# Optimization experiments

Measured on AMD Instinct MI355X. Metric: run time of the kernel, lower is better.

Reference implementation:

```python
import jax, jax.numpy as jnp
import numpy as np

WS = (8, 8)  # window_size
NUM_HEADS = 6


def _relative_position_index(ws):
    ch, cw = np.arange(ws[0]), np.arange(ws[1])
    coords = np.stack(np.meshgrid(ch, cw, indexing='ij'))  # [2, Wh, Ww]
    cf = coords.reshape(2, -1)  # [2, N]
    rel = cf[:, :, None] - cf[:, None, :]  # [2, N, N]
    rel = rel.transpose(1, 2, 0).astype(np.int64)
    rel[:, :, 0] += ws[0] - 1
    rel[:, :, 1] += ws[1] - 1
    rel[:, :, 0] *= 2 * ws[1] - 1
    return rel.sum(-1)  # [N, N]

_RPI = jnp.asarray(_relative_position_index(WS))  # [64, 64] int


def setup_inputs() -> dict:
    key = jax.random.key(0)
    ks = jax.random.split(key, 6)
    B_, N, C = 4096, WS[0] * WS[1], 192
    return {
        'x': jax.random.normal(ks[0], (B_, N, C), jnp.float32),
        'qkv_w': jax.random.normal(ks[1], (3 * C, C), jnp.float32) * 0.02,
        'qkv_b': jax.random.normal(ks[2], (3 * C,), jnp.float32) * 0.02,
        'proj_w': jax.random.normal(ks[3], (C, C), jnp.float32) * 0.02,
        'proj_b': jax.random.normal(ks[4], (C,), jnp.float32) * 0.02,
        'rpb_table': jax.random.normal(ks[5], ((2 * WS[0] - 1) * (2 * WS[1] - 1), NUM_HEADS), jnp.float32) * 0.02,
    }


def reference(x, qkv_w, qkv_b, proj_w, proj_b, rpb_table):
    B_, N, C = x.shape
    H = NUM_HEADS
    D = C // H
    scale = D ** (-0.5)
    # qkv: torch Linear -> x @ W^T + b
    qkv = (x @ qkv_w.T + qkv_b).reshape(B_, N, 3, H, D)
    qkv = jnp.transpose(qkv, (2, 0, 3, 1, 4))  # [3, B_, H, N, D]
    q, k, v = qkv[0] * scale, qkv[1], qkv[2]
    attn = jnp.einsum('bhnd,bhmd->bhnm', q, k)  # [B_, H, N, N]
    bias = rpb_table[_RPI]  # [N, N, H]
    attn = attn + jnp.transpose(bias, (2, 0, 1))[None]  # broadcast over B_
    attn = jax.nn.softmax(attn, axis=-1)
    out = jnp.einsum('bhnm,bhmd->bnhd', attn, v).reshape(B_, N, C)
    return out @ proj_w.T + proj_b
```

## Files before the change

kernel.cpp:

```cpp
#include <hip/hip_runtime.h>
#include <hip/hip_bf16.h>

typedef short bf16x8 __attribute__((ext_vector_type(8)));
typedef float f32x4 __attribute__((ext_vector_type(4)));
typedef unsigned int u32;
typedef unsigned int u32x2 __attribute__((ext_vector_type(2)));

#define MFMA16 __builtin_amdgcn_mfma_f32_16x16x32_bf16
#define SCALE 0.17677669529663687f

#define OS_OFF 395520
#define WS_NEED (395520 + 100663296)

__device__ __forceinline__ unsigned short f2b(float x) {
  u32 u = __float_as_uint(x);
  u = (u + 0x7FFFu + ((u >> 16) & 1u)) >> 16;
  return (unsigned short)u;
}
__device__ __forceinline__ u32 pk2(float a, float b) {
  __hip_bfloat162 h = __float22bfloat162_rn(float2{a, b});
  return *(u32*)&h;
}
__device__ __forceinline__ uint2 pk4(f32x4 v) {
  return make_uint2(pk2(v[0], v[1]), pk2(v[2], v[3]));
}

__device__ __forceinline__ bf16x8 xpose(f32x4 a0, f32x4 a1) {
  u32 s0 = pk2(a0[0], a0[1]);
  u32 s1 = pk2(a0[2], a0[3]);
  u32 s2 = pk2(a1[0], a1[1]);
  u32 s3 = pk2(a1[2], a1[3]);
  u32x2 r0 = __builtin_amdgcn_permlane16_swap(s0, s2, false, false);
  u32x2 r1 = __builtin_amdgcn_permlane16_swap(s1, s3, false, false);
  union {
    u32 w[4];
    bf16x8 v;
  } u;
  u.w[0] = r0[0];
  u.w[1] = r1[0];
  u.w[2] = r0[1];
  u.w[3] = r1[1];
  return u.v;
}

__global__ void prep_kernel(const float* __restrict__ qkv_w, const float* __restrict__ qkv_b,
                            const float* __restrict__ proj_w, const float* __restrict__ rpb,
                            unsigned short* __restrict__ wqkv, unsigned short* __restrict__ wproj,
                            float* __restrict__ biasar, float* __restrict__ bq) {
  int i0 = blockIdx.x * blockDim.x + threadIdx.x;
  int stride = gridDim.x * blockDim.x;
  for (int i = i0; i < 576 * 192; i += stride) {
    float v = qkv_w[i];
    if (i < 192 * 192) v *= SCALE;
    wqkv[i] = f2b(v);
  }
  for (int i = i0; i < 192 * 192; i += stride) wproj[i] = f2b(proj_w[i]);
  for (int i = i0; i < 576; i += stride) {
    float v = qkv_b[i];
    if (i < 192) v *= SCALE;
    bq[i] = v;
  }
  for (int i = i0; i < 6 * 16 * 64 * 4; i += stride) {
    int r = i & 3;
    int lane = (i >> 2) & 63;
    int fid = (i >> 8) & 15;
    int h = i >> 12;
    int mt = fid >> 2, nt = fid & 3;
    int m = mt * 16 + (lane >> 4) * 4 + r;
    int n = nt * 16 + (lane & 15);
    int idx = ((n >> 3) - (m >> 3) + 7) * 15 + ((n & 7) - (m & 7) + 7);
    biasar[i] = rpb[idx * 6 + h];
  }
}

__global__ void __launch_bounds__(384, 4) win_attn6(
    const float* __restrict__ x, const unsigned short* __restrict__ wqkv,
    const float* __restrict__ biasar, const float* __restrict__ bq,
    unsigned short* __restrict__ osout) {
  __shared__ __align__(16) char smem[50176];
  const int bid = blockIdx.x;
  const int b = bid >> 1;
  const int hg = bid & 1;
  const int tid = threadIdx.x;
  const int wv = tid >> 6;
  const int hl = wv >> 1;
  const int head = hg * 3 + hl;
  const int half = wv & 1;
  const int lane = tid & 63;
  const int g = lane >> 4;
  const int c = lane & 15;
  char* xs = smem;
  char* exch = smem + 25600;

  {
    const float4* src = (const float4*)(x + (size_t)b * 12288) + tid;
    char* wdst = xs + (tid / 48) * 400 + (tid % 48) * 8;
#pragma unroll
    for (int it = 0; it < 8; ++it) {
      float4 v = src[it * 384];
      *(uint2*)(wdst + it * 3200) = make_uint2(pk2(v.x, v.y), pk2(v.z, v.w));
    }
  }
  __syncthreads();

  const char* xr = xs + c * 400 + g * 16;
#define XF(tt, kt) (*(const bf16x8*)(xr + (tt) * 6400 + (kt) * 64))

  bf16x8 qb[2];
  {
    const unsigned short* wq0 = wqkv + (size_t)(head * 32 + c) * 192 + 8 * g;
    const unsigned short* wq1 = wq0 + 16 * 192;
    f32x4 bq0 = *(const f32x4*)(bq + head * 32 + 4 * g);
    f32x4 bq1 = *(const f32x4*)(bq + head * 32 + 16 + 4 * g);
    f32x4 a00 = bq0, a01 = bq0, a10 = bq1, a11 = bq1;
#pragma unroll
    for (int kt = 0; kt < 6; ++kt) {
      bf16x8 w0 = *(const bf16x8*)(wq0 + kt * 32);
      bf16x8 w1 = *(const bf16x8*)(wq1 + kt * 32);
      bf16x8 x0 = XF(half * 2 + 0, kt);
      bf16x8 x1 = XF(half * 2 + 1, kt);
      a00 = MFMA16(w0, x0, a00, 0, 0, 0);
      a10 = MFMA16(w1, x0, a10, 0, 0, 0);
      a01 = MFMA16(w0, x1, a01, 0, 0, 0);
      a11 = MFMA16(w1, x1, a11, 0, 0, 0);
    }
    qb[0] = xpose(a00, a10);
    qb[1] = xpose(a01, a11);
  }

  bf16x8 ka[4], va[2][2];
  {
    char* ew = exch + hl * 8192 + half * 4096 + lane * 16;
    if (half == 0) {
      const unsigned short* wk0 = wqkv + (size_t)(192 + head * 32 + c) * 192 + 8 * g;
      const unsigned short* wk1 = wk0 + 16 * 192;
      f32x4 bk0 = *(const f32x4*)(bq + 192 + head * 32 + 4 * g);
      f32x4 bk1 = *(const f32x4*)(bq + 192 + head * 32 + 16 + 4 * g);
      f32x4 acc[2][4];
#pragma unroll
      for (int tt = 0; tt < 4; ++tt) {
        acc[0][tt] = bk0;
        acc[1][tt] = bk1;
      }
#pragma unroll
      for (int kt = 0; kt < 6; ++kt) {
        bf16x8 w0 = *(const bf16x8*)(wk0 + kt * 32);
        bf16x8 w1 = *(const bf16x8*)(wk1 + kt * 32);
#pragma unroll
        for (int tt = 0; tt < 4; ++tt) {
          bf16x8 xf = XF(tt, kt);
          acc[0][tt] = MFMA16(w0, xf, acc[0][tt], 0, 0, 0);
          acc[1][tt] = MFMA16(w1, xf, acc[1][tt], 0, 0, 0);
        }
      }
#pragma unroll
      for (int mt = 0; mt < 4; ++mt) {
        ka[mt] = xpose(acc[0][mt], acc[1][mt]);
        *(bf16x8*)(ew + mt * 1024) = ka[mt];
      }
    } else {
      const unsigned short* wv0 = wqkv + (size_t)(384 + head * 32 + c) * 192 + 8 * g;
      const unsigned short* wv1 = wv0 + 16 * 192;
      float bv0 = bq[384 + head * 32 + c];
      float bv1 = bq[384 + head * 32 + 16 + c];
      f32x4 acc[4][2];
#pragma unroll
      for (int tt = 0; tt < 4; ++tt) {
        acc[tt][0] = f32x4{bv0, bv0, bv0, bv0};
        acc[tt][1] = f32x4{bv1, bv1, bv1, bv1};
      }
#pragma unroll
      for (int kt = 0; kt < 6; ++kt) {
        bf16x8 w0 = *(const bf16x8*)(wv0 + kt * 32);
        bf16x8 w1 = *(const bf16x8*)(wv1 + kt * 32);
#pragma unroll
        for (int tt = 0; tt < 4; ++tt) {
          bf16x8 xf = XF(tt, kt);
          acc[tt][0] = MFMA16(xf, w0, acc[tt][0], 0, 0, 0);
          acc[tt][1] = MFMA16(xf, w1, acc[tt][1], 0, 0, 0);
        }
      }
#pragma unroll
      for (int dt = 0; dt < 2; ++dt)
#pragma unroll
        for (int kh = 0; kh < 2; ++kh) {
          va[dt][kh] = xpose(acc[2 * kh][dt], acc[2 * kh + 1][dt]);
          *(bf16x8*)(ew + (dt * 2 + kh) * 1024) = va[dt][kh];
        }
    }
  }
  __syncthreads();
  {
    const char* er = exch + hl * 8192 + (half ^ 1) * 4096 + lane * 16;
    if (half == 0) {
#pragma unroll
      for (int f = 0; f < 4; ++f) va[f >> 1][f & 1] = *(const bf16x8*)(er + f * 1024);
    } else {
#pragma unroll
      for (int f = 0; f < 4; ++f) ka[f] = *(const bf16x8*)(er + f * 1024);
    }
  }

  bf16x8 pbf[2][2];
  float linv[2];
  {
    const f32x4* bias4 = (const f32x4*)biasar + (size_t)(head * 16 + half * 2) * 64 + lane;
    f32x4 s[4][2];
#pragma unroll
    for (int mt = 0; mt < 4; ++mt)
#pragma unroll
      for (int n2 = 0; n2 < 2; ++n2)
        s[mt][n2] = MFMA16(ka[mt], qb[n2], bias4[(mt * 4 + n2) * 64], 0, 0, 0);
#pragma unroll
    for (int n2 = 0; n2 < 2; ++n2) {
      float mx = fmaxf(fmaxf(fmaxf(s[0][n2][0], s[0][n2][1]), fmaxf(s[0][n2][2], s[0][n2][3])),
                       fmaxf(fmaxf(s[1][n2][0], s[1][n2][1]), fmaxf(s[1][n2][2], s[1][n2][3])));
      mx = fmaxf(mx, fmaxf(fmaxf(fmaxf(s[2][n2][0], s[2][n2][1]), fmaxf(s[2][n2][2], s[2][n2][3])),
                           fmaxf(fmaxf(s[3][n2][0], s[3][n2][1]), fmaxf(s[3][n2][2], s[3][n2][3]))));
      mx = fmaxf(mx, __shfl_xor(mx, 16));
      mx = fmaxf(mx, __shfl_xor(mx, 32));
      float sum = 0.0f;
#pragma unroll
      for (int mt = 0; mt < 4; ++mt)
#pragma unroll
        for (int r = 0; r < 4; ++r) {
          float e = __expf(s[mt][n2][r] - mx);
          s[mt][n2][r] = e;
          sum += e;
        }
      sum += __shfl_xor(sum, 16);
      sum += __shfl_xor(sum, 32);
      linv[n2] = 1.0f / sum;
    }
#pragma unroll
    for (int n2 = 0; n2 < 2; ++n2) {
      pbf[0][n2] = xpose(s[0][n2], s[1][n2]);
      pbf[1][n2] = xpose(s[2][n2], s[3][n2]);
    }
  }

  f32x4 o[2][2];
#pragma unroll
  for (int dt = 0; dt < 2; ++dt)
#pragma unroll
    for (int n2 = 0; n2 < 2; ++n2) o[dt][n2] = (f32x4)0.0f;
#pragma unroll
  for (int mh = 0; mh < 2; ++mh)
#pragma unroll
    for (int n2 = 0; n2 < 2; ++n2)
#pragma unroll
      for (int dt = 0; dt < 2; ++dt) o[dt][n2] = MFMA16(va[dt][mh], pbf[mh][n2], o[dt][n2], 0, 0, 0);

  uint2* dst = (uint2*)osout + ((size_t)((b * 6 + head) * 2 + half) * 4) * 64 + lane;
#pragma unroll
  for (int dt = 0; dt < 2; ++dt)
#pragma unroll
    for (int n2 = 0; n2 < 2; ++n2) {
#pragma unroll
      for (int r = 0; r < 4; ++r) o[dt][n2][r] *= linv[n2];
      dst[(dt * 2 + n2) * 64] = pk4(o[dt][n2]);
    }
}

__global__ void __launch_bounds__(256, 4) proj_kernel(
    const unsigned short* __restrict__ osin, const unsigned short* __restrict__ wproj,
    const float* __restrict__ proj_b, float* __restrict__ out) {
  __shared__ __align__(16) char smem[24576];
  const int b = blockIdx.x;
  const int tid = threadIdx.x;
  const int w = tid >> 6;
  const int lane = tid & 63;
  const int g = lane >> 4;
  const int c = lane & 15;

  {
    const uint2* src = (const uint2*)osin + (size_t)b * 3072;
#pragma unroll
    for (int it = 0; it < 12; ++it) {
      int i = tid + it * 256;
      int ls = i & 63;
      int f = (i >> 6) & 3;
      int unit = i >> 8;
      int head = unit >> 1, half = unit & 1;
      int dt = f >> 1, n2 = f & 1;
      int tok = half * 32 + n2 * 16 + (ls & 15);
      int d0 = head * 32 + dt * 16 + 4 * (ls >> 4);
      uint2 v = src[i];
      *(uint2*)(smem + tok * 384 + (((d0 >> 3) ^ (tok & 7)) << 4) + (d0 & 7) * 2) = v;
    }
  }
  __syncthreads();

  f32x4 acc[4][3];
#pragma unroll
  for (int mt = 0; mt < 4; ++mt)
#pragma unroll
    for (int ft = 0; ft < 3; ++ft) acc[mt][ft] = (f32x4)0.0f;
#pragma unroll
  for (int kt = 0; kt < 6; ++kt) {
    bf16x8 wf[3];
#pragma unroll
    for (int ft = 0; ft < 3; ++ft)
      wf[ft] = *(const bf16x8*)(wproj + (size_t)(w * 48 + ft * 16 + c) * 192 + kt * 32 + 8 * g);
#pragma unroll
    for (int mt = 0; mt < 4; ++mt) {
      bf16x8 of = *(const bf16x8*)(smem + (mt * 16 + c) * 384 + (((kt * 4 + g) ^ (c & 7)) << 4));
#pragma unroll
      for (int ft = 0; ft < 3; ++ft) acc[mt][ft] = MFMA16(of, wf[ft], acc[mt][ft], 0, 0, 0);
    }
  }
  float* outb = out + (size_t)b * 12288;
#pragma unroll
  for (int ft = 0; ft < 3; ++ft) {
    float pbv = proj_b[w * 48 + ft * 16 + c];
#pragma unroll
    for (int mt = 0; mt < 4; ++mt)
#pragma unroll
      for (int r = 0; r < 4; ++r)
        outb[(mt * 16 + 4 * g + r) * 192 + w * 48 + ft * 16 + c] = acc[mt][ft][r] + pbv;
  }
}

#define XFRAGOLD(tt, kt) \
  (*(const bf16x8*)(xs + ((tt) * 16 + c) * 384 + ((((kt) * 4 + g) ^ (c & 7)) << 4)))

__global__ void __launch_bounds__(384, 3) win_attn(
    const float* __restrict__ x, const unsigned short* __restrict__ wqkv,
    const unsigned short* __restrict__ wproj, const float* __restrict__ biasar,
    const float* __restrict__ bq, const float* __restrict__ proj_b, float* __restrict__ out) {
  __shared__ __align__(16) char smem[24576];
  const int b = blockIdx.x;
  const int tid = threadIdx.x;
  const int w = tid >> 6;
  const int lane = tid & 63;
  const int g = lane >> 4;
  const int c = lane & 15;
  char* xs = smem;

  {
    const float* xb = x + (size_t)b * 12288;
#pragma unroll
    for (int it = 0; it < 8; ++it) {
      int idx = tid + it * 384;
      int tok = idx / 48, c4 = idx % 48;
      float4 v = *(const float4*)(xb + tok * 192 + c4 * 4);
      *(uint2*)(xs + tok * 384 + (((c4 >> 1) ^ (tok & 7)) << 4) + (c4 & 1) * 8) =
          make_uint2(pk2(v.x, v.y), pk2(v.z, v.w));
    }
  }
  __syncthreads();

  bf16x8 qb[4];
  {
    f32x4 acc[2][4];
#pragma unroll
    for (int dt = 0; dt < 2; ++dt)
#pragma unroll
      for (int tt = 0; tt < 4; ++tt) acc[dt][tt] = (f32x4)0.0f;
#pragma unroll
    for (int kt = 0; kt < 6; ++kt) {
      bf16x8 wf[2];
#pragma unroll
      for (int dt = 0; dt < 2; ++dt)
        wf[dt] = *(const bf16x8*)(wqkv + (size_t)(w * 32 + dt * 16 + c) * 192 + kt * 32 + 8 * g);
#pragma unroll
      for (int tt = 0; tt < 4; ++tt) {
        bf16x8 xf = XFRAGOLD(tt, kt);
#pragma unroll
        for (int dt = 0; dt < 2; ++dt) acc[dt][tt] = MFMA16(wf[dt], xf, acc[dt][tt], 0, 0, 0);
      }
    }
#pragma unroll
    for (int dt = 0; dt < 2; ++dt)
#pragma unroll
      for (int r = 0; r < 4; ++r) {
        float bv = bq[w * 32 + dt * 16 + 4 * g + r];
#pragma unroll
        for (int tt = 0; tt < 4; ++tt) acc[dt][tt][r] += bv;
      }
#pragma unroll
    for (int nt = 0; nt < 4; ++nt) qb[nt] = xpose(acc[0][nt], acc[1][nt]);
  }

  bf16x8 ka[4];
  {
    f32x4 acc[2][4];
#pragma unroll
    for (int dt = 0; dt < 2; ++dt)
#pragma unroll
      for (int tt = 0; tt < 4; ++tt) acc[dt][tt] = (f32x4)0.0f;
#pragma unroll
    for (int kt = 0; kt < 6; ++kt) {
      bf16x8 wf[2];
#pragma unroll
      for (int dt = 0; dt < 2; ++dt)
        wf[dt] =
            *(const bf16x8*)(wqkv + (size_t)(192 + w * 32 + dt * 16 + c) * 192 + kt * 32 + 8 * g);
#pragma unroll
      for (int tt = 0; tt < 4; ++tt) {
        bf16x8 xf = XFRAGOLD(tt, kt);
#pragma unroll
        for (int dt = 0; dt < 2; ++dt) acc[dt][tt] = MFMA16(wf[dt], xf, acc[dt][tt], 0, 0, 0);
      }
    }
#pragma unroll
    for (int dt = 0; dt < 2; ++dt)
#pragma unroll
      for (int r = 0; r < 4; ++r) {
        float bv = bq[192 + w * 32 + dt * 16 + 4 * g + r];
#pragma unroll
        for (int tt = 0; tt < 4; ++tt) acc[dt][tt][r] += bv;
      }
#pragma unroll
    for (int mt = 0; mt < 4; ++mt) ka[mt] = xpose(acc[0][mt], acc[1][mt]);
  }

  bf16x8 pbf[2][4];
  float linv[4];
  const f32x4* bias4 = (const f32x4*)biasar;
#pragma unroll
  for (int h = 0; h < 2; ++h) {
    f32x4 s[4][2];
#pragma unroll
    for (int mt = 0; mt < 4; ++mt)
#pragma unroll
      for (int n2 = 0; n2 < 2; ++n2) {
        int nt = h * 2 + n2;
        f32x4 t = MFMA16(ka[mt], qb[nt], (f32x4)0.0f, 0, 0, 0);
        s[mt][n2] = t + bias4[(w * 16 + mt * 4 + nt) * 64 + lane];
      }
#pragma unroll
    for (int n2 = 0; n2 < 2; ++n2) {
      int nt = h * 2 + n2;
      float mx = -1e30f;
#pragma unroll
      for (int mt = 0; mt < 4; ++mt)
#pragma unroll
        for (int r = 0; r < 4; ++r) mx = fmaxf(mx, s[mt][n2][r]);
      mx = fmaxf(mx, __shfl_xor(mx, 16));
      mx = fmaxf(mx, __shfl_xor(mx, 32));
      float sum = 0.0f;
#pragma unroll
      for (int mt = 0; mt < 4; ++mt)
#pragma unroll
        for (int r = 0; r < 4; ++r) {
          float e = __expf(s[mt][n2][r] - mx);
          s[mt][n2][r] = e;
          sum += e;
        }
      sum += __shfl_xor(sum, 16);
      sum += __shfl_xor(sum, 32);
      linv[nt] = 1.0f / sum;
    }
#pragma unroll
    for (int n2 = 0; n2 < 2; ++n2) {
      pbf[0][h * 2 + n2] = xpose(s[0][n2], s[1][n2]);
      pbf[1][h * 2 + n2] = xpose(s[2][n2], s[3][n2]);
    }
  }

  bf16x8 va[2][2];
  {
    f32x4 acc[4][2];
#pragma unroll
    for (int mt = 0; mt < 4; ++mt)
#pragma unroll
      for (int dt = 0; dt < 2; ++dt) acc[mt][dt] = (f32x4)0.0f;
#pragma unroll
    for (int kt = 0; kt < 6; ++kt) {
      bf16x8 wf[2];
#pragma unroll
      for (int dt = 0; dt < 2; ++dt)
        wf[dt] =
            *(const bf16x8*)(wqkv + (size_t)(384 + w * 32 + dt * 16 + c) * 192 + kt * 32 + 8 * g);
#pragma unroll
      for (int tt = 0; tt < 4; ++tt) {
        bf16x8 xf = XFRAGOLD(tt, kt);
#pragma unroll
        for (int dt = 0; dt < 2; ++dt) acc[tt][dt] = MFMA16(xf, wf[dt], acc[tt][dt], 0, 0, 0);
      }
    }
#pragma unroll
    for (int dt = 0; dt < 2; ++dt) {
      float bv = bq[384 + w * 32 + dt * 16 + c];
#pragma unroll
      for (int mt = 0; mt < 4; ++mt)
#pragma unroll
        for (int r = 0; r < 4; ++r) acc[mt][dt][r] += bv;
    }
#pragma unroll
    for (int dt = 0; dt < 2; ++dt)
#pragma unroll
      for (int kh = 0; kh < 2; ++kh) va[dt][kh] = xpose(acc[2 * kh][dt], acc[2 * kh + 1][dt]);
  }

  f32x4 o[2][4];
#pragma unroll
  for (int dt = 0; dt < 2; ++dt)
#pragma unroll
    for (int nt = 0; nt < 4; ++nt) o[dt][nt] = (f32x4)0.0f;
#pragma unroll
  for (int mh = 0; mh < 2; ++mh)
#pragma unroll
    for (int nt = 0; nt < 4; ++nt)
#pragma unroll
      for (int dt = 0; dt < 2; ++dt) o[dt][nt] = MFMA16(va[dt][mh], pbf[mh][nt], o[dt][nt], 0, 0, 0);
#pragma unroll
  for (int dt = 0; dt < 2; ++dt)
#pragma unroll
    for (int nt = 0; nt < 4; ++nt)
#pragma unroll
      for (int r = 0; r < 4; ++r) o[dt][nt][r] *= linv[nt];

  __syncthreads();
#pragma unroll
  for (int dt = 0; dt < 2; ++dt)
#pragma unroll
    for (int nt = 0; nt < 4; ++nt)
      *(uint2*)(xs + (nt * 16 + c) * 384 + (((w * 4 + dt * 2 + (g >> 1)) ^ (c & 7)) << 4) +
                (g & 1) * 8) =
          make_uint2(pk2(o[dt][nt][0], o[dt][nt][1]), pk2(o[dt][nt][2], o[dt][nt][3]));
  __syncthreads();

  f32x4 accP[4][2];
#pragma unroll
  for (int mt = 0; mt < 4; ++mt)
#pragma unroll
    for (int ft = 0; ft < 2; ++ft) accP[mt][ft] = (f32x4)0.0f;
#pragma unroll
  for (int kt = 0; kt < 6; ++kt) {
    bf16x8 wp[2];
#pragma unroll
    for (int ft = 0; ft < 2; ++ft)
      wp[ft] = *(const bf16x8*)(wproj + (size_t)(w * 32 + ft * 16 + c) * 192 + kt * 32 + 8 * g);
#pragma unroll
    for (int mt = 0; mt < 4; ++mt) {
      bf16x8 of = *(const bf16x8*)(xs + (mt * 16 + c) * 384 + (((kt * 4 + g) ^ (c & 7)) << 4));
#pragma unroll
      for (int ft = 0; ft < 2; ++ft) accP[mt][ft] = MFMA16(of, wp[ft], accP[mt][ft], 0, 0, 0);
    }
  }
  float pb0 = proj_b[w * 32 + c];
  float pb1 = proj_b[w * 32 + 16 + c];
  float* outb = out + (size_t)b * 12288;
#pragma unroll
  for (int mt = 0; mt < 4; ++mt)
#pragma unroll
    for (int ft = 0; ft < 2; ++ft) {
      float pbv = ft ? pb1 : pb0;
#pragma unroll
      for (int r = 0; r < 4; ++r)
        outb[(mt * 16 + 4 * g + r) * 192 + w * 32 + ft * 16 + c] = accP[mt][ft][r] + pbv;
    }
}

extern "C" void kernel_launch(void* const* d_in, const int* in_sizes, int n_in,
                              void* d_out, int out_size, void* d_ws, size_t ws_size,
                              hipStream_t stream) {
  const float* x = (const float*)d_in[0];
  const float* qkv_w = (const float*)d_in[1];
  const float* qkv_b = (const float*)d_in[2];
  const float* proj_w = (const float*)d_in[3];
  const float* proj_b = (const float*)d_in[4];
  const float* rpb = (const float*)d_in[5];
  char* ws = (char*)d_ws;
  unsigned short* wqkv = (unsigned short*)ws;
  unsigned short* wproj = (unsigned short*)(ws + 221184);
  float* biasar = (float*)(ws + 294912);
  float* bqv = (float*)(ws + 393216);

  prep_kernel<<<432, 256, 0, stream>>>(qkv_w, qkv_b, proj_w, rpb, wqkv, wproj, biasar, bqv);

  if (ws_size >= (size_t)WS_NEED) {
    unsigned short* osbuf = (unsigned short*)(ws + OS_OFF);
    win_attn6<<<8192, 384, 0, stream>>>(x, wqkv, biasar, bqv, osbuf);
    proj_kernel<<<4096, 256, 0, stream>>>(osbuf, wproj, proj_b, (float*)d_out);
  } else {
    win_attn<<<4096, 384, 0, stream>>>(x, wqkv, wproj, biasar, bqv, proj_b, (float*)d_out);
  }
}
```

Baseline: 317.1 us.

## Fuse Q into K/V projection loops, swizzle x tile, use exp2 and setprio

Merges the separate Q projection loop into the K and V projection loops so each x fragment read from LDS is reused for both. It also swaps the padded x tile layout for an XOR-swizzled 384-byte-stride layout to avoid bank conflicts and shrink LDS. LOG2E is folded into the Q weights, Q bias and relative bias so softmax can use exp2 directly. s_setprio hints are placed around the MFMA sections. These are several loosely related changes to LDS traffic, instruction count and scheduling, and the larger fused loop raises register pressure.

```diff
diff --git a/kernel.cpp b/kernel.cpp
--- a/kernel.cpp
+++ b/kernel.cpp
@@ -8,6 +8,7 @@
 
 #define MFMA16 __builtin_amdgcn_mfma_f32_16x16x32_bf16
 #define SCALE 0.17677669529663687f
+#define LOG2E 1.4426950408889634f
 
 #define OS_OFF 395520
 #define WS_NEED (395520 + 100663296)
@@ -51,13 +52,13 @@
   int stride = gridDim.x * blockDim.x;
   for (int i = i0; i < 576 * 192; i += stride) {
     float v = qkv_w[i];
-    if (i < 192 * 192) v *= SCALE;
+    if (i < 192 * 192) v *= SCALE * LOG2E;
     wqkv[i] = f2b(v);
   }
   for (int i = i0; i < 192 * 192; i += stride) wproj[i] = f2b(proj_w[i]);
   for (int i = i0; i < 576; i += stride) {
     float v = qkv_b[i];
-    if (i < 192) v *= SCALE;
+    if (i < 192) v *= SCALE * LOG2E;
     bq[i] = v;
   }
   for (int i = i0; i < 6 * 16 * 64 * 4; i += stride) {
@@ -69,7 +70,7 @@
     int m = mt * 16 + (lane >> 4) * 4 + r;
     int n = nt * 16 + (lane & 15);
     int idx = ((n >> 3) - (m >> 3) + 7) * 15 + ((n & 7) - (m & 7) + 7);
-    biasar[i] = rpb[idx * 6 + h];
+    biasar[i] = rpb[idx * 6 + h] * LOG2E;
   }
 }
 
@@ -77,7 +78,7 @@
     const float* __restrict__ x, const unsigned short* __restrict__ wqkv,
     const float* __restrict__ biasar, const float* __restrict__ bq,
     unsigned short* __restrict__ osout) {
-  __shared__ __align__(16) char smem[50176];
+  __shared__ __align__(16) char smem[49152];
   const int bid = blockIdx.x;
   const int b = bid >> 1;
   const int hg = bid & 1;
@@ -90,72 +91,76 @@
   const int g = lane >> 4;
   const int c = lane & 15;
   char* xs = smem;
-  char* exch = smem + 25600;
-
-  {
-    const float4* src = (const float4*)(x + (size_t)b * 12288) + tid;
-    char* wdst = xs + (tid / 48) * 400 + (tid % 48) * 8;
+  char* exch = smem + 24576;
+
+  {
+    const float* xb = x + (size_t)b * 12288;
 #pragma unroll
     for (int it = 0; it < 8; ++it) {
-      float4 v = src[it * 384];
-      *(uint2*)(wdst + it * 3200) = make_uint2(pk2(v.x, v.y), pk2(v.z, v.w));
+      int idx = tid + it * 384;
+      int tok = idx / 48, c4 = idx % 48;
+      float4 v = *(const float4*)(xb + tok * 192 + c4 * 4);
+      *(uint2*)(xs + tok * 384 + (((c4 >> 1) ^ (tok & 7)) << 4) + (c4 & 1) * 8) =
+          make_uint2(pk2(v.x, v.y), pk2(v.z, v.w));
     }
   }
   __syncthreads();
 
-  const char* xr = xs + c * 400 + g * 16;
-#define XF(tt, kt) (*(const bf16x8*)(xr + (tt) * 6400 + (kt) * 64))
-
-  bf16x8 qb[2];
+#define XF(tt, kt) \
+  (*(const bf16x8*)(xs + ((tt) * 16 + c) * 384 + ((((kt) * 4 + g) ^ (c & 7)) << 4)))
+
+  bf16x8 qb[2], ka[4], va[2][2];
   {
     const unsigned short* wq0 = wqkv + (size_t)(head * 32 + c) * 192 + 8 * g;
     const unsigned short* wq1 = wq0 + 16 * 192;
     f32x4 bq0 = *(const f32x4*)(bq + head * 32 + 4 * g);
     f32x4 bq1 = *(const f32x4*)(bq + head * 32 + 16 + 4 * g);
-    f32x4 a00 = bq0, a01 = bq0, a10 = bq1, a11 = bq1;
-#pragma unroll
-    for (int kt = 0; kt < 6; ++kt) {
-      bf16x8 w0 = *(const bf16x8*)(wq0 + kt * 32);
-      bf16x8 w1 = *(const bf16x8*)(wq1 + kt * 32);
-      bf16x8 x0 = XF(half * 2 + 0, kt);
-      bf16x8 x1 = XF(half * 2 + 1, kt);
-      a00 = MFMA16(w0, x0, a00, 0, 0, 0);
-      a10 = MFMA16(w1, x0, a10, 0, 0, 0);
-      a01 = MFMA16(w0, x1, a01, 0, 0, 0);
-      a11 = MFMA16(w1, x1, a11, 0, 0, 0);
-    }
-    qb[0] = xpose(a00, a10);
-    qb[1] = xpose(a01, a11);
-  }
-
-  bf16x8 ka[4], va[2][2];
-  {
+    f32x4 aq[2][2];
+    aq[0][0] = bq0;
+    aq[0][1] = bq0;
+    aq[1][0] = bq1;
+    aq[1][1] = bq1;
     char* ew = exch + hl * 8192 + half * 4096 + lane * 16;
     if (half == 0) {
       const unsigned short* wk0 = wqkv + (size_t)(192 + head * 32 + c) * 192 + 8 * g;
       const unsigned short* wk1 = wk0 + 16 * 192;
       f32x4 bk0 = *(const f32x4*)(bq + 192 + head * 32 + 4 * g);
       f32x4 bk1 = *(const f32x4*)(bq + 192 + head * 32 + 16 + 4 * g);
-      f32x4 acc[2][4];
+      f32x4 ak[2][4];
 #pragma unroll
       for (int tt = 0; tt < 4; ++tt) {
-        acc[0][tt] = bk0;
-        acc[1][tt] = bk1;
-      }
+        ak[0][tt] = bk0;
+        ak[1][tt] = bk1;
+      }
+      __builtin_amdgcn_s_setprio(1);
 #pragma unroll
       for (int kt = 0; kt < 6; ++kt) {
-        bf16x8 w0 = *(const bf16x8*)(wk0 + kt * 32);
-        bf16x8 w1 = *(const bf16x8*)(wk1 + kt * 32);
-#pragma unroll
-        for (int tt = 0; tt < 4; ++tt) {
-          bf16x8 xf = XF(tt, kt);
-          acc[0][tt] = MFMA16(w0, xf, acc[0][tt], 0, 0, 0);
-          acc[1][tt] = MFMA16(w1, xf, acc[1][tt], 0, 0, 0);
-        }
-      }
+        bf16x8 xf0 = XF(0, kt), xf1 = XF(1, kt), xf2 = XF(2, kt), xf3 = XF(3, kt);
+        bf16x8 q0 = *(const bf16x8*)(wq0 + kt * 32);
+        bf16x8 q1 = *(const bf16x8*)(wq1 + kt * 32);
+        bf16x8 k0 = *(const bf16x8*)(wk0 + kt * 32);
+        bf16x8 k1 = *(const bf16x8*)(wk1 + kt * 32);
+        bf16x8 xq0 = half ? xf2 : xf0;
+        bf16x8 xq1 = half ? xf3 : xf1;
+        aq[0][0] = MFMA16(q0, xq0, aq[0][0], 0, 0, 0);
+        aq[1][0] = MFMA16(q1, xq0, aq[1][0], 0, 0, 0);
+        aq[0][1] = MFMA16(q0, xq1, aq[0][1], 0, 0, 0);
+        aq[1][1] = MFMA16(q1, xq1, aq[1][1], 0, 0, 0);
+        ak[0][0] = MFMA16(k0, xf0, ak[0][0], 0, 0, 0);
+        ak[1][0] = MFMA16(k1, xf0, ak[1][0], 0, 0, 0);
+        ak[0][1] = MFMA16(k0, xf1, ak[0][1], 0, 0, 0);
+        ak[1][1] = MFMA16(k1, xf1, ak[1][1], 0, 0, 0);
+        ak[0][2] = MFMA16(k0, xf2, ak[0][2], 0, 0, 0);
+        ak[1][2] = MFMA16(k1, xf2, ak[1][2], 0, 0, 0);
+        ak[0][3] = MFMA16(k0, xf3, ak[0][3], 0, 0, 0);
+        ak[1][3] = MFMA16(k1, xf3, ak[1][3], 0, 0, 0);
+      }
+      __builtin_amdgcn_s_setprio(0);
+      qb[0] = xpose(aq[0][0], aq[1][0]);
+      qb[1] = xpose(aq[0][1], aq[1][1]);
 #pragma unroll
       for (int mt = 0; mt < 4; ++mt) {
-        ka[mt] = xpose(acc[0][mt], acc[1][mt]);
+        ka[mt] = xpose(ak[0][mt], ak[1][mt]);
         *(bf16x8*)(ew + mt * 1024) = ka[mt];
       }
     } else {
@@ -163,28 +168,43 @@
       const unsigned short* wv1 = wv0 + 16 * 192;
       float bv0 = bq[384 + head * 32 + c];
       float bv1 = bq[384 + head * 32 + 16 + c];
-      f32x4 acc[4][2];
+      f32x4 av[4][2];
 #pragma unroll
       for (int tt = 0; tt < 4; ++tt) {
-        acc[tt][0] = f32x4{bv0, bv0, bv0, bv0};
-        acc[tt][1] = f32x4{bv1, bv1, bv1, bv1};
-      }
+        av[tt][0] = f32x4{bv0, bv0, bv0, bv0};
+        av[tt][1] = f32x4{bv1, bv1, bv1, bv1};
+      }
+      __builtin_amdgcn_s_setprio(1);
 #pragma unroll
       for (int kt = 0; kt < 6; ++kt) {
-        bf16x8 w0 = *(const bf16x8*)(wv0 + kt * 32);
-        bf16x8 w1 = *(const bf16x8*)(wv1 + kt * 32);
-#pragma unroll
-        for (int tt = 0; tt < 4; ++tt) {
-          bf16x8 xf = XF(tt, kt);
-          acc[tt][0] = MFMA16(xf, w0, acc[tt][0], 0, 0, 0);
-          acc[tt][1] = MFMA16(xf, w1, acc[tt][1], 0, 0, 0);
-        }
-      }
+        bf16x8 xf0 = XF(0, kt), xf1 = XF(1, kt), xf2 = XF(2, kt), xf3 = XF(3, kt);
+        bf16x8 q0 = *(const bf16x8*)(wq0 + kt * 32);
+        bf16x8 q1 = *(const bf16x8*)(wq1 + kt * 32);
+        bf16x8 v0 = *(const bf16x8*)(wv0 + kt * 32);
+        bf16x8 v1 = *(const bf16x8*)(wv1 + kt * 32);
+        bf16x8 xq0 = half ? xf2 : xf0;
+        bf16x8 xq1 = half ? xf3 : xf1;
+        aq[0][0] = MFMA16(q0, xq0, aq[0][0], 0, 0, 0);
+        aq[1][0] = MFMA16(q1, xq0, aq[1][0], 0, 0, 0);
+        aq[0][1] = MFMA16(q0, xq1, aq[0][1], 0, 0, 0);
+        aq[1][1] = MFMA16(q1, xq1, aq[1][1], 0, 0, 0);
+        av[0][0] = MFMA16(xf0, v0, av[0][0], 0, 0, 0);
+        av[0][1] = MFMA16(xf0, v1, av[0][1], 0, 0, 0);
+        av[1][0] = MFMA16(xf1, v0, av[1][0], 0, 0, 0);
+        av[1][1] = MFMA16(xf1, v1, av[1][1], 0, 0, 0);
+        av[2][0] = MFMA16(xf2, v0, av[2][0], 0, 0, 0);
+        av[2][1] = MFMA16(xf2, v1, av[2][1], 0, 0, 0);
+        av[3][0] = MFMA16(xf3, v0, av[3][0], 0, 0, 0);
+        av[3][1] = MFMA16(xf3, v1, av[3][1], 0, 0, 0);
+      }
+      __builtin_amdgcn_s_setprio(0);
+      qb[0] = xpose(aq[0][0], aq[1][0]);
+      qb[1] = xpose(aq[0][1], aq[1][1]);
 #pragma unroll
       for (int dt = 0; dt < 2; ++dt)
 #pragma unroll
         for (int kh = 0; kh < 2; ++kh) {
-          va[dt][kh] = xpose(acc[2 * kh][dt], acc[2 * kh + 1][dt]);
+          va[dt][kh] = xpose(av[2 * kh][dt], av[2 * kh + 1][dt]);
           *(bf16x8*)(ew + (dt * 2 + kh) * 1024) = va[dt][kh];
         }
     }
@@ -206,11 +226,13 @@
   {
     const f32x4* bias4 = (const f32x4*)biasar + (size_t)(head * 16 + half * 2) * 64 + lane;
     f32x4 s[4][2];
+    __builtin_amdgcn_s_setprio(1);
 #pragma unroll
     for (int mt = 0; mt < 4; ++mt)
 #pragma unroll
       for (int n2 = 0; n2 < 2; ++n2)
         s[mt][n2] = MFMA16(ka[mt], qb[n2], bias4[(mt * 4 + n2) * 64], 0, 0, 0);
+    __builtin_amdgcn_s_setprio(0);
 #pragma unroll
     for (int n2 = 0; n2 < 2; ++n2) {
       float mx = fmaxf(fmaxf(fmaxf(s[0][n2][0], s[0][n2][1]), fmaxf(s[0][n2][2], s[0][n2][3])),
@@ -224,7 +246,7 @@
       for (int mt = 0; mt < 4; ++mt)
 #pragma unroll
         for (int r = 0; r < 4; ++r) {
-          float e = __expf(s[mt][n2][r] - mx);
+          float e = __builtin_exp2f(s[mt][n2][r] - mx);
           s[mt][n2][r] = e;
           sum += e;
         }
@@ -244,12 +266,14 @@
   for (int dt = 0; dt < 2; ++dt)
 #pragma unroll
     for (int n2 = 0; n2 < 2; ++n2) o[dt][n2] = (f32x4)0.0f;
+  __builtin_amdgcn_s_setprio(1);
 #pragma unroll
   for (int mh = 0; mh < 2; ++mh)
 #pragma unroll
     for (int n2 = 0; n2 < 2; ++n2)
 #pragma unroll
       for (int dt = 0; dt < 2; ++dt) o[dt][n2] = MFMA16(va[dt][mh], pbf[mh][n2], o[dt][n2], 0, 0, 0);
+  __builtin_amdgcn_s_setprio(0);
 
   uint2* dst = (uint2*)osout + ((size_t)((b * 6 + head) * 2 + half) * 4) * 64 + lane;
 #pragma unroll
@@ -444,7 +468,7 @@
       for (int mt = 0; mt < 4; ++mt)
 #pragma unroll
         for (int r = 0; r < 4; ++r) {
-          float e = __expf(s[mt][n2][r] - mx);
+          float e = __builtin_exp2f(s[mt][n2][r] - mx);
           s[mt][n2][r] = e;
           sum += e;
         }
```

Measured after the change: 335.0 us. 1.06x slower.
